# Kernel optimization log

Hardware: AMD Instinct MI355X
Metric: run time of the kernel (lower is better)

The kernel has to match this reference:

```python
import jax, jax.numpy as jnp
import numpy as np

NMS_PRE, NMS_POST, NMS_THRESH = 1024, 512, 0.7
B, A, FEAT = 4, 70400, 27648
BN_EPS = 1e-5


def _bev_iou(boxes):
    # boxes: [K, 7] (x, y, z, dx, dy, dz, ry); axis-aligned BEV IoU
    x, y, dx, dy = boxes[:, 0], boxes[:, 1], boxes[:, 3], boxes[:, 4]
    x1, x2 = x - 0.5 * dx, x + 0.5 * dx
    y1, y2 = y - 0.5 * dy, y + 0.5 * dy
    iw = jnp.clip(jnp.minimum(x2[:, None], x2[None, :]) - jnp.maximum(x1[:, None], x1[None, :]), 0.0)
    ih = jnp.clip(jnp.minimum(y2[:, None], y2[None, :]) - jnp.maximum(y1[:, None], y1[None, :]), 0.0)
    inter = iw * ih
    area = dx * dy
    return inter / jnp.clip(area[:, None] + area[None, :] - inter, 1e-6)


def _greedy_nms(boxes, thresh):
    # boxes sorted by score desc; returns keep mask [K]
    K = boxes.shape[0]
    iou = _bev_iou(boxes)
    idx = jnp.arange(K)

    def step(keep, i):
        sup = (iou[i] > thresh) & (idx > i) & keep[i]
        return keep & ~sup, None

    keep, _ = jax.lax.scan(step, jnp.ones(K, dtype=bool), jnp.arange(K))
    return keep


def _proposal_one(box, cls):
    # box: [A, 7], cls: [A, n_cls]  ->  padded rois [NPOST,7], scores [NPOST], labels [NPOST]
    score = jnp.max(cls, axis=-1)
    label = jnp.argmax(cls, axis=-1)
    top_score, top_idx = jax.lax.top_k(score, NMS_PRE)
    top_box = box[top_idx]
    keep = _greedy_nms(top_box, NMS_THRESH)
    # stable: kept entries first, preserving score order
    order = jnp.argsort(jnp.where(keep, jnp.arange(NMS_PRE), NMS_PRE + jnp.arange(NMS_PRE)))
    sel = order[:NMS_POST]
    valid = jnp.arange(NMS_POST) < jnp.minimum(jnp.sum(keep), NMS_POST)
    rois = jnp.where(valid[:, None], top_box[sel], 0.0)
    roi_score = jnp.where(valid, top_score[sel], 0.0)
    roi_label = jnp.where(valid, label[top_idx][sel], 0) + 1  # +1 as in module
    return rois, roi_score, roi_label


def _bn_relu(h, g, b):
    # eval-mode BN with running_mean=0, running_var=1
    return jax.nn.relu(h * (g / jnp.sqrt(1.0 + BN_EPS)) + b)


def _decode(reg, anchors):
    # ResidualCoder_v1.decode_torch
    xa, ya, za = anchors[..., 0], anchors[..., 1], anchors[..., 2]
    dxa, dya, dza, ra = anchors[..., 3], anchors[..., 4], anchors[..., 5], anchors[..., 6]
    xt, yt, zt = reg[..., 0], reg[..., 1], reg[..., 2]
    dxt, dyt, dzt, rt = reg[..., 3], reg[..., 4], reg[..., 5], reg[..., 6]
    diag = jnp.sqrt(dxa * dxa + dya * dya)
    return jnp.stack([
        xt * diag + xa, yt * diag + ya, zt * dza + za,
        jnp.exp(dxt) * dxa, jnp.exp(dyt) * dya, jnp.exp(dzt) * dza,
        rt + ra], axis=-1)


def _rotate_z(box, ang):
    # rotate x,y of box [..., 7] by ang [...]
    c, s = jnp.cos(ang), jnp.sin(ang)
    x = box[..., 0] * c - box[..., 1] * s
    y = box[..., 0] * s + box[..., 1] * c
    return jnp.concatenate([x[..., None], y[..., None], box[..., 2:]], axis=-1)


def reference(rpn_box_preds, rpn_cls_preds, pooled_features,
              Ws1, g1, b1, Ws2, g2, b2,
              Wc1, gc1, bc1, Wc2, gc2, bc2, Wc3, bc3,
              Wr1, gr1, br1, Wr2, gr2, br2, Wr3, br3):
    # proposal_layer: per-batch topk + NMS + padded scatter (vmapped)
    rois, roi_scores, roi_labels = jax.vmap(_proposal_one)(rpn_box_preds, rpn_cls_preds)

    # shared / cls / reg heads (1x1 Conv1d == per-roi MLP), dropout off (eval)
    x = _bn_relu(pooled_features @ Ws1.T, g1, b1)
    x = _bn_relu(x @ Ws2.T, g2, b2)
    c = _bn_relu(x @ Wc1.T, gc1, bc1)
    c = _bn_relu(c @ Wc2.T, gc2, bc2)
    cls_preds = c @ Wc3.T + bc3          # [B*NPOST, 1]
    r = _bn_relu(x @ Wr1.T, gr1, br1)
    r = _bn_relu(r @ Wr2.T, gr2, br2)
    reg_preds = r @ Wr3.T + br3          # [B*NPOST, 7]

    bsz = rois.shape[0]
    cls_preds = cls_preds.reshape(bsz, -1, cls_preds.shape[-1])
    reg_preds = reg_preds.reshape(bsz, -1, 7)

    # generate_predict_box: decode against detached rois with xyz zeroed
    anchors = jax.lax.stop_gradient(rois)
    anchors = anchors.at[..., 0:3].set(0.0)
    box_ct = _decode(reg_preds, anchors)
    box_preds = _rotate_z(box_ct, rois[..., 6])
    box_preds = jnp.concatenate([box_preds[..., 0:3] + rois[..., 0:3], box_preds[..., 3:]], axis=-1)

    return jnp.concatenate([cls_preds, box_preds, roi_scores[..., None]], axis=-1)  # [B, NPOST, 9]


def setup_inputs():
    key = jax.random.key(0)
    ks = jax.random.split(key, 32)
    u = jax.random.uniform(ks[0], (B, A, 7), dtype=jnp.float32)
    lo = jnp.array([0.0, -40.0, -2.0, 1.5, 1.4, 1.0, -3.14159], jnp.float32)
    hi = jnp.array([70.0, 40.0, 0.0, 4.5, 2.0, 2.0, 3.14159], jnp.float32)
    rpn_box_preds = lo + u * (hi - lo)
    rpn_cls_preds = jax.random.normal(ks[1], (B, A, 3), dtype=jnp.float32)
    pooled_features = jax.random.normal(ks[2], (B * NMS_POST, FEAT), dtype=jnp.float32) * 0.1

    def w(k, o, i, std=None):
        s = (1.0 / np.sqrt(i)) if std is None else std
        return jax.random.normal(k, (o, i), dtype=jnp.float32) * s

    d = dict(
        rpn_box_preds=rpn_box_preds, rpn_cls_preds=rpn_cls_preds, pooled_features=pooled_features,
        Ws1=w(ks[3], 256, FEAT), g1=jnp.ones(256), b1=jnp.zeros(256),
        Ws2=w(ks[4], 256, 256), g2=jnp.ones(256), b2=jnp.zeros(256),
        Wc1=w(ks[5], 256, 256), gc1=jnp.ones(256), bc1=jnp.zeros(256),
        Wc2=w(ks[6], 256, 256), gc2=jnp.ones(256), bc2=jnp.zeros(256),
        Wc3=w(ks[7], 1, 256), bc3=jnp.zeros(1),
        Wr1=w(ks[8], 256, 256), gr1=jnp.ones(256), br1=jnp.zeros(256),
        Wr2=w(ks[9], 256, 256), gr2=jnp.ones(256), br2=jnp.zeros(256),
        Wr3=w(ks[10], 7, 256, std=0.001), br3=jnp.zeros(7),
    )
    return d
```

## Files before the change

kernel.cpp:

```cpp
#include <hip/hip_runtime.h>
#include <cstdint>

typedef unsigned int u32;
typedef unsigned long long u64;
typedef unsigned short u16;

#define BATCH 4
#define A_CNT 70400
#define FEAT 27648
#define KSPLIT 16
#define KCHUNK 1728
#define NTILE_IT 27

typedef __attribute__((ext_vector_type(8))) short bf16x8;
typedef __attribute__((ext_vector_type(4))) float f32x4;
typedef __attribute__((ext_vector_type(2))) u32 u32x2;
typedef __attribute__((ext_vector_type(4))) u32 u32x4;

constexpr size_t OF_KEYS = 0;
constexpr size_t OF_TBOX = OF_KEYS + 1126400;
constexpr size_t OF_TSC  = OF_TBOX + 114688;
constexpr size_t OF_BX1  = OF_TSC + 16384;
constexpr size_t OF_BX2  = OF_BX1 + 16384;
constexpr size_t OF_BY1  = OF_BX2 + 16384;
constexpr size_t OF_BY2  = OF_BY1 + 16384;
constexpr size_t OF_BAR  = OF_BY2 + 16384;
constexpr size_t OF_MASK = OF_BAR + 16384;
constexpr size_t OF_ROIS = OF_MASK + 524288;
constexpr size_t OF_RSC  = OF_ROIS + 57344;
constexpr size_t OF_BSW  = OF_RSC + 8192;
constexpr size_t OF_PART = OF_BSW + 14155776;
constexpr size_t WS_NEED = OF_PART + 33554432;

__device__ __forceinline__ u32 keyOf(float f) {
  u32 u = __float_as_uint(f);
  return (u & 0x80000000u) ? ~u : (u | 0x80000000u);
}
__device__ __forceinline__ float keyToF(u32 k) {
  u32 u = (k & 0x80000000u) ? (k ^ 0x80000000u) : ~k;
  return __uint_as_float(u);
}
__device__ __forceinline__ u16 f2bf(float f) {
  u32 u = __float_as_uint(f);
  u32 r = 0x7FFFu + ((u >> 16) & 1u);
  return (u16)((u + r) >> 16);
}
__device__ __forceinline__ void gload_lds16(const void* g, void* l) {
  auto gp = reinterpret_cast<const __attribute__((address_space(1))) unsigned int*>(
      reinterpret_cast<uintptr_t>(g));
  auto lp = reinterpret_cast<__attribute__((address_space(3))) unsigned int*>(
      reinterpret_cast<uintptr_t>(l));
  __builtin_amdgcn_global_load_lds(gp, lp, 16, 0, 0);
}
__device__ __forceinline__ u64 shflx64(u64 v, int m) {
  u32 lo = (u32)v, hi = (u32)(v >> 32);
  lo = __shfl_xor(lo, m, 64);
  hi = __shfl_xor(hi, m, 64);
  return ((u64)hi << 32) | lo;
}
__device__ __forceinline__ u32x4 pack8(float4 a, float4 b) {
  u32x4 o;
  o.x = (u32)f2bf(a.x) | ((u32)f2bf(a.y) << 16);
  o.y = (u32)f2bf(a.z) | ((u32)f2bf(a.w) << 16);
  o.z = (u32)f2bf(b.x) | ((u32)f2bf(b.y) << 16);
  o.w = (u32)f2bf(b.z) | ((u32)f2bf(b.w) << 16);
  return o;
}

__global__ __launch_bounds__(1024) void k_fatA(const float* __restrict__ cls,
    const float* __restrict__ Ws1, u32* __restrict__ keys, u32* __restrict__ Bsw)
{
  int bid = blockIdx.x;
  int t = threadIdx.x;
  if (bid < 864) {
    u32 w = (u32)bid * 1024u + t;
    u32 tile = w >> 11;
    u32 rem = w & 2047u;
    u32 n = rem >> 3;
    u32 pq = (rem & 7u) << 4;
    u32 q0 = pq ^ ((n & 7u) << 4);
    u32 col0 = tile * 64u + (q0 >> 1);
    const float* src = Ws1 + (size_t)n * FEAT + col0;
    float4 f0 = *(const float4*)src;
    float4 f1 = *(const float4*)(src + 4);
    ((u32x4*)Bsw)[w] = pack8(f0, f1);
    return;
  }
  u32 g = (u32)(bid - 864) * 1024u + t;
  float s0 = cls[(size_t)g * 3 + 0];
  float s1 = cls[(size_t)g * 3 + 1];
  float s2 = cls[(size_t)g * 3 + 2];
  keys[g] = keyOf(fmaxf(s0, fmaxf(s1, s2)));
}

__global__ __launch_bounds__(1024) void k_big(const u32* __restrict__ keys,
    const float* __restrict__ boxes, const float* __restrict__ A,
    const u32* __restrict__ Bsw, float* __restrict__ part,
    float* __restrict__ tbox, float* __restrict__ tsc,
    float* __restrict__ bx1, float* __restrict__ bx2, float* __restrict__ by1,
    float* __restrict__ by2, float* __restrict__ bar)
{
  __shared__ __align__(16) char smem[98304];
  int bid = blockIdx.x;
  int t = threadIdx.x;
  if (bid < 4) {
    int b = bid;
    int lane = t & 63, wv = t >> 6;
    const u32* kb = keys + (size_t)b * A_CNT;
    u64* s = (u64*)smem;
    u32* partials = (u32*)(smem + 16384);
    u32* ccp = (u32*)(smem + 16448);
    u32 h[35];
#pragma unroll
    for (int j = 0; j < 35; ++j) {
      int g0 = t + ((2 * j) << 10);
      int g1 = t + ((2 * j + 1) << 10);
      u32 a = (g0 < A_CNT) ? (kb[g0] >> 16) : 0u;
      u32 c2 = (g1 < A_CNT) ? (kb[g1] >> 16) : 0u;
      h[j] = a | (c2 << 16);
    }
    if (t == 0) ccp[0] = 0u;
    u32 lo = 0, hi = 65536;
    while (hi - lo > 1) {
      u32 mid = (lo + hi) >> 1;
      u32 c = 0;
#pragma unroll
      for (int j = 0; j < 35; ++j) {
        c += ((h[j] & 0xFFFFu) >= mid) ? 1u : 0u;
        c += ((h[j] >> 16) >= mid) ? 1u : 0u;
      }
#pragma unroll
      for (int o = 32; o > 0; o >>= 1) c += __shfl_xor(c, o, 64);
      __syncthreads();
      if (lane == 0) partials[wv] = c;
      __syncthreads();
      u32 tot = 0;
#pragma unroll
      for (int w2 = 0; w2 < 16; ++w2) tot += partials[w2];
      if (tot >= 1024u) lo = mid; else hi = mid;
    }
    u32 kth = lo;
    __syncthreads();
    u32 kc = kb[t];
#pragma unroll 1
    for (int i = 0; i < 69; ++i) {
      int g = t + (i << 10);
      u32 k = kc;
      if (i < 68) {
        int gn = t + ((i + 1) << 10);
        kc = (gn < A_CNT) ? kb[gn] : 0u;
      }
      bool pass = (g < A_CNT) && ((k >> 16) >= kth);
      u64 mm = __ballot(pass);
      if (mm) {
        int leader = __ffsll((unsigned long long)mm) - 1;
        u32 base = 0;
        if (lane == leader) base = atomicAdd(ccp, (u32)__popcll(mm));
        base = __shfl(base, leader, 64);
        if (pass) {
          u32 pos = base + (u32)__popcll(mm & ((1ull << lane) - 1ull));
          if (pos < 2048u) s[pos] = ((u64)k << 32) | (u32)(~(u32)g);
        }
      }
    }
    __syncthreads();
    u32 m = ccp[0]; if (m > 2048u) m = 2048u;
    for (int e = t; e < 2048; e += 1024) if (e >= (int)m) s[e] = 0ull;
    __syncthreads();
    {
      u64 v0 = s[2 * t], v1 = s[2 * t + 1];
#pragma unroll
      for (u32 k = 2; k <= 128; k <<= 1) {
        bool desc = ((t & (k >> 1)) == 0);
#pragma unroll
        for (u32 j = (k >> 1); j >= 2; j >>= 1) {
          u32 mmk = j >> 1;
          u64 p0 = shflx64(v0, mmk);
          u64 p1 = shflx64(v1, mmk);
          bool up = ((t & mmk) == 0);
          bool mx = (desc == up);
          v0 = mx ? (v0 > p0 ? v0 : p0) : (v0 < p0 ? v0 : p0);
          v1 = mx ? (v1 > p1 ? v1 : p1) : (v1 < p1 ? v1 : p1);
        }
        if (desc ? (v0 < v1) : (v0 > v1)) { u64 tmp = v0; v0 = v1; v1 = tmp; }
      }
      s[2 * t] = v0; s[2 * t + 1] = v1;
      __syncthreads();
      for (u32 k = 256; k <= 2048; k <<= 1) {
        for (u32 j = k >> 1; j >= 128; j >>= 1) {
          for (int e = t; e < 2048; e += 1024) {
            u32 p = (u32)e ^ j;
            if (p > (u32)e) {
              bool d2 = ((e & k) == 0);
              u64 x = s[e], y = s[p];
              if (d2 ? (x < y) : (x > y)) { s[e] = y; s[p] = x; }
            }
          }
          __syncthreads();
        }
        u64 v0 = s[2 * t], v1 = s[2 * t + 1];
        bool desc = ((t & (k >> 1)) == 0);
#pragma unroll
        for (u32 j = 64; j >= 2; j >>= 1) {
          u32 mmk = j >> 1;
          u64 p0 = shflx64(v0, mmk);
          u64 p1 = shflx64(v1, mmk);
          bool up = ((t & mmk) == 0);
          bool mx = (desc == up);
          v0 = mx ? (v0 > p0 ? v0 : p0) : (v0 < p0 ? v0 : p0);
          v1 = mx ? (v1 > p1 ? v1 : p1) : (v1 < p1 ? v1 : p1);
        }
        if (desc ? (v0 < v1) : (v0 > v1)) { u64 tmp = v0; v0 = v1; v1 = tmp; }
        s[2 * t] = v0; s[2 * t + 1] = v1;
        __syncthreads();
      }
    }
    u64 comp = s[t];
    u32 kk = (u32)(comp >> 32);
    u32 a = ~(u32)(comp & 0xFFFFFFFFull);
    int o = b * 1024 + t;
    tsc[o] = keyToF(kk);
    const float* bp = boxes + ((size_t)b * A_CNT + a) * 7;
    float x = bp[0], y = bp[1], z = bp[2], dx = bp[3], dy = bp[4], dz = bp[5], rr = bp[6];
    float* tb = tbox + (size_t)o * 7;
    tb[0] = x; tb[1] = y; tb[2] = z; tb[3] = dx; tb[4] = dy; tb[5] = dz; tb[6] = rr;
    {
#pragma clang fp contract(off)
      bx1[o] = x - 0.5f * dx; bx2[o] = x + 0.5f * dx;
      by1[o] = y - 0.5f * dy; by2[o] = y + 0.5f * dy;
      bar[o] = dx * dy;
    }
    return;
  }
  int bid2 = bid - 4;
  int q = bid2 >> 3;
  int ks = (bid2 & 7) * 2 + (q >> 4);
  int mt = q & 15;
  int lane = t & 63, wvid = t >> 6;
  int row16 = lane & 15, kgrp = lane >> 4;
  int gm = wvid >> 2, gn = wvid & 3;

  f32x4 acc[2][4];
#pragma unroll
  for (int i = 0; i < 2; ++i)
#pragma unroll
    for (int j = 0; j < 4; ++j) acc[i][j] = (f32x4){0.f, 0.f, 0.f, 0.f};

  int arow = t >> 3;
  const float* ap_base = A + ((size_t)(mt * 128 + arow)) * FEAT + (size_t)ks * KCHUNK + (t & 7) * 8;
  int asw = (arow & 7) << 4;
  int awoff = arow * 128 + (((t & 7) * 16) ^ asw);
  const char* bsrc_base = (const char*)Bsw + ((size_t)(ks * NTILE_IT)) * 32768 + wvid * 2048 + lane * 16;
  int bdoff = wvid * 2048 + lane * 16;
  char* Abase = smem;
  char* Bbase = smem + 32768;

  int aoff[2][2], boff[4][2];
#pragma unroll
  for (int ksub = 0; ksub < 2; ++ksub) {
    int qq = ksub * 64 + kgrp * 16;
#pragma unroll
    for (int mf = 0; mf < 2; ++mf) {
      int row = gm * 32 + mf * 16 + row16;
      aoff[mf][ksub] = row * 128 + (qq ^ ((row & 7) << 4));
    }
#pragma unroll
    for (int nf = 0; nf < 4; ++nf) {
      int n = gn * 64 + nf * 16 + row16;
      boff[nf][ksub] = n * 128 + (qq ^ ((n & 7) << 4));
    }
  }

  {
    const float4* ap = (const float4*)ap_base;
    float4 ga0 = ap[0], ga1 = ap[1];
    *(u32x4*)(Abase + awoff) = pack8(ga0, ga1);
    gload_lds16(bsrc_base, Bbase + bdoff);
    gload_lds16(bsrc_base + 1024, Bbase + bdoff + 1024);
  }
  __syncthreads();

  for (int it = 0; it < NTILE_IT; ++it) {
    char* Acur = Abase + ((it & 1) ? 16384 : 0);
    char* Anxt = Abase + ((it & 1) ? 0 : 16384);
    char* Bcur = Bbase + ((it & 1) ? 32768 : 0);
    char* Bnxt = Bbase + ((it & 1) ? 0 : 32768);
    bool has = (it + 1 < NTILE_IT);
    float4 ga0, ga1;
    if (has) {
      const float4* ap = (const float4*)(ap_base + (it + 1) * 64);
      ga0 = ap[0]; ga1 = ap[1];
      const char* bs = bsrc_base + (size_t)(it + 1) * 32768;
      gload_lds16(bs, Bnxt + bdoff);
      gload_lds16(bs + 1024, Bnxt + bdoff + 1024);
    }
    bf16x8 af[2][2], bf[4][2];
#pragma unroll
    for (int ksub = 0; ksub < 2; ++ksub) {
#pragma unroll
      for (int mf = 0; mf < 2; ++mf) af[mf][ksub] = *(const bf16x8*)(Acur + aoff[mf][ksub]);
#pragma unroll
      for (int nf = 0; nf < 4; ++nf) bf[nf][ksub] = *(const bf16x8*)(Bcur + boff[nf][ksub]);
    }
#pragma unroll
    for (int ksub = 0; ksub < 2; ++ksub)
#pragma unroll
      for (int mf = 0; mf < 2; ++mf)
#pragma unroll
        for (int nf = 0; nf < 4; ++nf)
          acc[mf][nf] = __builtin_amdgcn_mfma_f32_16x16x32_bf16(af[mf][ksub], bf[nf][ksub], acc[mf][nf], 0, 0, 0);
    if (has)
      *(u32x4*)(Anxt + awoff) = pack8(ga0, ga1);
    __syncthreads();
  }
  float* pb = part + (size_t)ks * 524288;
#pragma unroll
  for (int mf = 0; mf < 2; ++mf) {
    int orow = mt * 128 + gm * 32 + mf * 16 + kgrp * 4;
#pragma unroll
    for (int nf = 0; nf < 4; ++nf) {
      int col = gn * 64 + nf * 16 + row16;
#pragma unroll
      for (int rr = 0; rr < 4; ++rr)
        pb[(size_t)(orow + rr) * 256 + col] = acc[mf][nf][rr];
    }
  }
}

__global__ __launch_bounds__(1024) void k_mask(const float* __restrict__ bx1,
    const float* __restrict__ bx2, const float* __restrict__ by1,
    const float* __restrict__ by2, const float* __restrict__ bar,
    u32* __restrict__ mask)
{
  __shared__ float csm[16][5][64];
  int tt = threadIdx.x;
  int ug = tt >> 6, ln = tt & 63;
  int unit = blockIdx.x * 16 + ug;
  int b = unit >> 8, cbk = (unit >> 4) & 15, rb = unit & 15;
  int o = b * 1024, jc0 = cbk * 64;
  int r = rb * 64 + ln;
  csm[ug][0][ln] = bx1[o + jc0 + ln];
  csm[ug][1][ln] = bx2[o + jc0 + ln];
  csm[ug][2][ln] = by1[o + jc0 + ln];
  csm[ug][3][ln] = by2[o + jc0 + ln];
  csm[ug][4][ln] = bar[o + jc0 + ln];
  __syncthreads();
  float rx1 = bx1[o + r], rx2 = bx2[o + r], ry1 = by1[o + r], ry2 = by2[o + r], rar = bar[o + r];
  u32 w0 = 0, w1 = 0;
  {
#pragma clang fp contract(off)
    for (int c = 0; c < 64; ++c) {
      int jc = jc0 + c;
      float iw = fminf(rx2, csm[ug][1][c]) - fmaxf(rx1, csm[ug][0][c]); iw = fmaxf(iw, 0.0f);
      float ih = fminf(ry2, csm[ug][3][c]) - fmaxf(ry1, csm[ug][2][c]); ih = fmaxf(ih, 0.0f);
      float inter = iw * ih;
      float den = fmaxf(rar + csm[ug][4][c] - inter, 1e-6f);
      float iou = inter / den;
      if ((iou > 0.7f) && (jc > r)) {
        if (c < 32) w0 |= 1u << c; else w1 |= 1u << (c - 32);
      }
    }
  }
  mask[((size_t)(o + r)) * 32 + cbk * 2 + 0] = w0;
  mask[((size_t)(o + r)) * 32 + cbk * 2 + 1] = w1;
}

__global__ __launch_bounds__(64) void k_nms(const u32* __restrict__ mask,
    const float* __restrict__ tbox, const float* __restrict__ tsc,
    float* __restrict__ rois, float* __restrict__ rsc)
{
  int b = blockIdx.x;
  int lane = threadIdx.x;
  int el = lane & 31;
  const u32* M = mask + (size_t)b * 1024 * 32;
  u32 R = 0;
  u32 cur[32], nxt[32];
#pragma unroll
  for (int i = 0; i < 32; ++i) cur[i] = M[(size_t)(i * 32 + el)];
#pragma unroll 1
  for (int c = 0; c < 32; ++c) {
    if (c < 31) {
      int nb = (c + 1) * 1024 + el;
#pragma unroll
      for (int i = 0; i < 32; ++i) nxt[i] = M[(size_t)(nb + i * 32)];
    }
    u32 w = R;
#pragma unroll
    for (int i = 0; i < 32; ++i) w |= ((w >> i) & 1u) ? 0u : cur[i];
    u32 wfin = __shfl(w, c, 64);
#pragma unroll
    for (int i = 0; i < 32; ++i) R |= ((wfin >> i) & 1u) ? 0u : cur[i];
#pragma unroll
    for (int i = 0; i < 32; ++i) cur[i] = nxt[i];
  }
  u32 keepw = (lane < 32) ? ~R : 0u;
  int c = __popc(keepw);
  int pre = c;
  for (int d = 1; d < 64; d <<= 1) {
    int v = __shfl_up(pre, d, 64);
    if (lane >= d) pre += v;
  }
  int total = __shfl(pre, 31, 64);
  int base = pre - c;
  if (lane < 32) {
    u32 w = keepw;
    int rank = base;
    while (w) {
      int bit = __ffs(w) - 1;
      w &= w - 1;
      if (rank < 512) {
        int r = lane * 32 + bit;
        const float* tb = tbox + ((size_t)b * 1024 + r) * 7;
        float* rp = rois + ((size_t)b * 512 + rank) * 7;
        rp[0] = tb[0]; rp[1] = tb[1]; rp[2] = tb[2]; rp[3] = tb[3];
        rp[4] = tb[4]; rp[5] = tb[5]; rp[6] = tb[6];
        rsc[b * 512 + rank] = tsc[b * 1024 + r];
      }
      rank++;
    }
  }
  for (int z = total + lane; z < 512; z += 64) {
    float* rp = rois + ((size_t)b * 512 + z) * 7;
    rp[0] = rp[1] = rp[2] = rp[3] = rp[4] = rp[5] = rp[6] = 0.0f;
    rsc[b * 512 + z] = 0.0f;
  }
}

__device__ __forceinline__ void layer4(const float (*IN)[256], const float* __restrict__ W,
    const float* __restrict__ g, const float* __restrict__ bb, float (*OUT)[256], int t, int h)
{
  float acc[4] = {0, 0, 0, 0};
  const float* Wrow = W + (size_t)t * 256;
  for (int k = 0; k < 256; k += 4) {
    float4 w4 = *(const float4*)&Wrow[k];
#pragma unroll
    for (int r = 0; r < 4; ++r) {
      float4 xv = *(const float4*)&IN[h * 4 + r][k];
      acc[r] = fmaf(xv.x, w4.x, acc[r]);
      acc[r] = fmaf(xv.y, w4.y, acc[r]);
      acc[r] = fmaf(xv.z, w4.z, acc[r]);
      acc[r] = fmaf(xv.w, w4.w, acc[r]);
    }
  }
  float sc = g[t] / sqrtf(1.0f + 1e-5f);
  float bv = bb[t];
#pragma unroll
  for (int r = 0; r < 4; ++r)
    OUT[h * 4 + r][t] = fmaxf(fmaf(acc[r], sc, bv), 0.0f);
}

__global__ __launch_bounds__(512) void k_chain(const float* __restrict__ part,
    const float* __restrict__ Ws2, const float* __restrict__ Wc1, const float* __restrict__ Wc2,
    const float* __restrict__ Wr1, const float* __restrict__ Wr2,
    const float* __restrict__ g1, const float* __restrict__ b1,
    const float* __restrict__ g2, const float* __restrict__ b2,
    const float* __restrict__ gc1, const float* __restrict__ bc1,
    const float* __restrict__ gc2, const float* __restrict__ bc2,
    const float* __restrict__ gr1, const float* __restrict__ br1,
    const float* __restrict__ gr2, const float* __restrict__ br2,
    const float* __restrict__ Wc3, const float* __restrict__ bc3,
    const float* __restrict__ Wr3, const float* __restrict__ br3,
    const float* __restrict__ rois, const float* __restrict__ rsc,
    float* __restrict__ out)
{
  int bid = blockIdx.x, tid = threadIdx.x;
  int t = tid & 255, h = tid >> 8;
  __shared__ __align__(16) float bufX[8][256];
  __shared__ __align__(16) float bufY[8][256];
  __shared__ __align__(16) float bufC[8][256];
  __shared__ __align__(16) float bufR[8][256];
  __shared__ float hd[64];
  {
    float sc = g1[t] / sqrtf(1.0f + 1e-5f);
    float bv = b1[t];
#pragma unroll
    for (int r = 0; r < 4; ++r) {
      int row = h * 4 + r;
      float s = 0.f;
#pragma unroll
      for (int ks = 0; ks < KSPLIT; ++ks)
        s += part[(size_t)ks * 524288 + (size_t)(bid * 8 + row) * 256 + t];
      bufX[row][t] = fmaxf(fmaf(s, sc, bv), 0.0f);
    }
  }
  __syncthreads();
  layer4(bufX, Ws2, g2, b2, bufY, t, h);
  __syncthreads();
  layer4(bufY, Wc1, gc1, bc1, bufC, t, h);
  layer4(bufY, Wr1, gr1, br1, bufR, t, h);
  __syncthreads();
  layer4(bufC, Wc2, gc2, bc2, bufX, t, h);
  layer4(bufR, Wr2, gr2, br2, bufY, t, h);
  __syncthreads();
  int wv = tid >> 6, ln = tid & 63;
  for (int task = wv; task < 64; task += 8) {
    float p;
    if (task < 8) {
      float4 yv = *(const float4*)&bufX[task][ln * 4];
      float4 w4 = ((const float4*)Wc3)[ln];
      p = yv.x * w4.x + yv.y * w4.y + yv.z * w4.z + yv.w * w4.w;
    } else {
      int i = task - 8, row = i / 7, j = i % 7;
      float4 yv = *(const float4*)&bufY[row][ln * 4];
      float4 w4 = ((const float4*)(Wr3 + j * 256))[ln];
      p = yv.x * w4.x + yv.y * w4.y + yv.z * w4.z + yv.w * w4.w;
    }
#pragma unroll
    for (int off = 32; off > 0; off >>= 1) p += __shfl_xor(p, off, 64);
    if (ln == 0) hd[task] = p;
  }
  __syncthreads();
  if (tid < 8) {
    int m = bid * 8 + tid;
    float clsv = hd[tid] + bc3[0];
    float rg[7];
#pragma unroll
    for (int j = 0; j < 7; ++j) rg[j] = hd[8 + tid * 7 + j] + br3[j];
    const float* R = rois + (size_t)m * 7;
    float rx = R[0], ry = R[1], rz = R[2], dxa = R[3], dya = R[4], dza = R[5], ra = R[6];
    float diag = sqrtf(dxa * dxa + dya * dya);
    float x = rg[0] * diag, y = rg[1] * diag, z = rg[2] * dza;
    float ex = expf(rg[3]) * dxa, ey = expf(rg[4]) * dya, ez = expf(rg[5]) * dza;
    float hr = rg[6] + ra;
    float cc = cosf(ra), sn = sinf(ra);
    float xr = x * cc - y * sn, yr = x * sn + y * cc;
    float* O = out + (size_t)m * 9;
    O[0] = clsv; O[1] = xr + rx; O[2] = yr + ry; O[3] = z + rz;
    O[4] = ex; O[5] = ey; O[6] = ez; O[7] = hr; O[8] = rsc[m];
  }
}

extern "C" void kernel_launch(void* const* d_in, const int* in_sizes, int n_in,
                              void* d_out, int out_size, void* d_ws, size_t ws_size,
                              hipStream_t stream)
{
  const float* rpn_box = (const float*)d_in[0];
  const float* rpn_cls = (const float*)d_in[1];
  const float* pooled  = (const float*)d_in[2];
  const float* Ws1 = (const float*)d_in[3];
  const float* g1  = (const float*)d_in[4];
  const float* b1  = (const float*)d_in[5];
  const float* Ws2 = (const float*)d_in[6];
  const float* g2  = (const float*)d_in[7];
  const float* b2  = (const float*)d_in[8];
  const float* Wc1 = (const float*)d_in[9];
  const float* gc1 = (const float*)d_in[10];
  const float* bc1 = (const float*)d_in[11];
  const float* Wc2 = (const float*)d_in[12];
  const float* gc2 = (const float*)d_in[13];
  const float* bc2 = (const float*)d_in[14];
  const float* Wc3 = (const float*)d_in[15];
  const float* bc3 = (const float*)d_in[16];
  const float* Wr1 = (const float*)d_in[17];
  const float* gr1 = (const float*)d_in[18];
  const float* br1 = (const float*)d_in[19];
  const float* Wr2 = (const float*)d_in[20];
  const float* gr2 = (const float*)d_in[21];
  const float* br2 = (const float*)d_in[22];
  const float* Wr3 = (const float*)d_in[23];
  const float* br3 = (const float*)d_in[24];

  if (ws_size < WS_NEED) return;

  char* ws = (char*)d_ws;
  u32* keys = (u32*)(ws + OF_KEYS);
  float* tbox = (float*)(ws + OF_TBOX);
  float* tsc  = (float*)(ws + OF_TSC);
  float* bx1 = (float*)(ws + OF_BX1);
  float* bx2 = (float*)(ws + OF_BX2);
  float* by1 = (float*)(ws + OF_BY1);
  float* by2 = (float*)(ws + OF_BY2);
  float* bar = (float*)(ws + OF_BAR);
  u32* mask = (u32*)(ws + OF_MASK);
  float* roisb = (float*)(ws + OF_ROIS);
  float* rscb  = (float*)(ws + OF_RSC);
  u32* Bsw = (u32*)(ws + OF_BSW);
  float* part = (float*)(ws + OF_PART);

  k_fatA<<<1139, 1024, 0, stream>>>(rpn_cls, Ws1, keys, Bsw);
  k_big<<<260, 1024, 0, stream>>>(keys, rpn_box, pooled, Bsw, part,
                                  tbox, tsc, bx1, bx2, by1, by2, bar);
  k_mask<<<64, 1024, 0, stream>>>(bx1, bx2, by1, by2, bar, mask);
  k_nms<<<4, 64, 0, stream>>>(mask, tbox, tsc, roisb, rscb);
  k_chain<<<256, 512, 0, stream>>>(part, Ws2, Wc1, Wc2, Wr1, Wr2,
                                   g1, b1, g2, b2, gc1, bc1, gc2, bc2,
                                   gr1, br1, gr2, br2, Wc3, bc3, Wr3, br3,
                                   roisb, rscb, (float*)d_out);
}
```

Measured before the change: 247.2 us.

## Triple-buffer B tiles with prefetch distance two and ping-pong NMS mask buffers

The split-K GEMM loop now prefetches the B tile two iterations ahead into a triple-buffered LDS region (shared memory grown to 128 KB). It replaces __syncthreads with explicit waitcnt on vmcnt and lgkmcnt plus s_barrier, so later loads stay in flight across the barrier. The NMS chunk loop is unrolled by two with ping-pong register buffers, removing the 32-element copy, and splits the OR reduction into four independent chains. The larger LDS footprint may reduce occupancy, and the hand-written waitcnt counts must match the real number of outstanding loads or the results will be wrong.

After: 242.7 us (median of 2 runs). No clear change (-1.8%).

```diff
diff --git a/kernel.cpp b/kernel.cpp
--- a/kernel.cpp
+++ b/kernel.cpp
@@ -100,7 +100,7 @@
     float* __restrict__ bx1, float* __restrict__ bx2, float* __restrict__ by1,
     float* __restrict__ by2, float* __restrict__ bar)
 {
-  __shared__ __align__(16) char smem[98304];
+  __shared__ __align__(16) char smem[131072];
   int bid = blockIdx.x;
   int t = threadIdx.x;
   if (bid < 4) {
@@ -271,28 +271,37 @@
     }
   }
 
+  float4 gaold0, gaold1;
   {
-    const float4* ap = (const float4*)ap_base;
-    float4 ga0 = ap[0], ga1 = ap[1];
-    *(u32x4*)(Abase + awoff) = pack8(ga0, ga1);
+    const float4* ap0 = (const float4*)ap_base;
+    float4 a00 = ap0[0], a01 = ap0[1];
     gload_lds16(bsrc_base, Bbase + bdoff);
     gload_lds16(bsrc_base + 1024, Bbase + bdoff + 1024);
-  }
-  __syncthreads();
-
+    const float4* ap1 = (const float4*)(ap_base + 64);
+    gaold0 = ap1[0]; gaold1 = ap1[1];
+    const char* bs1 = bsrc_base + 32768;
+    gload_lds16(bs1, Bbase + 32768 + bdoff);
+    gload_lds16(bs1 + 1024, Bbase + 32768 + bdoff + 1024);
+    *(u32x4*)(Abase + awoff) = pack8(a00, a01);
+    asm volatile("s_waitcnt lgkmcnt(0)" ::: "memory");
+    asm volatile("s_waitcnt vmcnt(4)" ::: "memory");
+    __builtin_amdgcn_sched_barrier(0);
+    __builtin_amdgcn_s_barrier();
+  }
+
+#pragma unroll 1
   for (int it = 0; it < NTILE_IT; ++it) {
-    char* Acur = Abase + ((it & 1) ? 16384 : 0);
-    char* Anxt = Abase + ((it & 1) ? 0 : 16384);
-    char* Bcur = Bbase + ((it & 1) ? 32768 : 0);
-    char* Bnxt = Bbase + ((it & 1) ? 0 : 32768);
-    bool has = (it + 1 < NTILE_IT);
-    float4 ga0, ga1;
-    if (has) {
-      const float4* ap = (const float4*)(ap_base + (it + 1) * 64);
-      ga0 = ap[0]; ga1 = ap[1];
-      const char* bs = bsrc_base + (size_t)(it + 1) * 32768;
-      gload_lds16(bs, Bnxt + bdoff);
-      gload_lds16(bs + 1024, Bnxt + bdoff + 1024);
+    char* Acur = Abase + ((it & 1) << 14);
+    char* Bcur = Bbase + (it % 3) * 32768;
+    bool pf = (it + 2 < NTILE_IT);
+    float4 gn0, gn1;
+    if (pf) {
+      const float4* ap = (const float4*)(ap_base + (it + 2) * 64);
+      gn0 = ap[0]; gn1 = ap[1];
+      const char* bs = bsrc_base + (size_t)(it + 2) * 32768;
+      char* Bn = Bbase + ((it + 2) % 3) * 32768;
+      gload_lds16(bs, Bn + bdoff);
+      gload_lds16(bs + 1024, Bn + bdoff + 1024);
     }
     bf16x8 af[2][2], bf[4][2];
 #pragma unroll
@@ -309,9 +318,16 @@
 #pragma unroll
         for (int nf = 0; nf < 4; ++nf)
           acc[mf][nf] = __builtin_amdgcn_mfma_f32_16x16x32_bf16(af[mf][ksub], bf[nf][ksub], acc[mf][nf], 0, 0, 0);
-    if (has)
-      *(u32x4*)(Anxt + awoff) = pack8(ga0, ga1);
-    __syncthreads();
+    if (it + 1 < NTILE_IT) {
+      char* An = Abase + (((it + 1) & 1) << 14);
+      *(u32x4*)(An + awoff) = pack8(gaold0, gaold1);
+      gaold0 = gn0; gaold1 = gn1;
+      asm volatile("s_waitcnt lgkmcnt(0)" ::: "memory");
+      if (pf) asm volatile("s_waitcnt vmcnt(4)" ::: "memory");
+      else    asm volatile("s_waitcnt vmcnt(0)" ::: "memory");
+      __builtin_amdgcn_sched_barrier(0);
+      __builtin_amdgcn_s_barrier();
+    }
   }
   float* pb = part + (size_t)ks * 524288;
 #pragma unroll
@@ -365,6 +381,27 @@
   mask[((size_t)(o + r)) * 32 + cbk * 2 + 1] = w1;
 }
 
+#define CHUNK_STEP(CUR, NXT, C) do {                                            \
+    if ((C) + 1 < 32) {                                                         \
+      int nb = ((C) + 1) * 1024 + el;                                           \
+      _Pragma("unroll")                                                         \
+      for (int i = 0; i < 32; ++i) NXT[i] = M[(size_t)(nb + i * 32)];           \
+    }                                                                           \
+    u32 w = R;                                                                  \
+    _Pragma("unroll")                                                           \
+    for (int i = 0; i < 32; ++i) w |= ((w >> i) & 1u) ? 0u : CUR[i];            \
+    u32 wfin = __shfl(w, (C), 64);                                              \
+    u32 m0 = 0, m1 = 0, m2 = 0, m3 = 0;                                         \
+    _Pragma("unroll")                                                           \
+    for (int i = 0; i < 32; i += 4) {                                           \
+      m0 |= ((wfin >> (i + 0)) & 1u) ? 0u : CUR[i + 0];                         \
+      m1 |= ((wfin >> (i + 1)) & 1u) ? 0u : CUR[i + 1];                         \
+      m2 |= ((wfin >> (i + 2)) & 1u) ? 0u : CUR[i + 2];                         \
+      m3 |= ((wfin >> (i + 3)) & 1u) ? 0u : CUR[i + 3];                         \
+    }                                                                           \
+    R |= (m0 | m1) | (m2 | m3);                                                 \
+  } while (0)
+
 __global__ __launch_bounds__(64) void k_nms(const u32* __restrict__ mask,
     const float* __restrict__ tbox, const float* __restrict__ tsc,
     float* __restrict__ rois, float* __restrict__ rsc)
@@ -374,24 +411,13 @@
   int el = lane & 31;
   const u32* M = mask + (size_t)b * 1024 * 32;
   u32 R = 0;
-  u32 cur[32], nxt[32];
-#pragma unroll
-  for (int i = 0; i < 32; ++i) cur[i] = M[(size_t)(i * 32 + el)];
+  u32 bufA[32], bufB[32];
+#pragma unroll
+  for (int i = 0; i < 32; ++i) bufA[i] = M[(size_t)(i * 32 + el)];
 #pragma unroll 1
-  for (int c = 0; c < 32; ++c) {
-    if (c < 31) {
-      int nb = (c + 1) * 1024 + el;
-#pragma unroll
-      for (int i = 0; i < 32; ++i) nxt[i] = M[(size_t)(nb + i * 32)];
-    }
-    u32 w = R;
-#pragma unroll
-    for (int i = 0; i < 32; ++i) w |= ((w >> i) & 1u) ? 0u : cur[i];
-    u32 wfin = __shfl(w, c, 64);
-#pragma unroll
-    for (int i = 0; i < 32; ++i) R |= ((wfin >> i) & 1u) ? 0u : cur[i];
-#pragma unroll
-    for (int i = 0; i < 32; ++i) cur[i] = nxt[i];
+  for (int c = 0; c < 32; c += 2) {
+    CHUNK_STEP(bufA, bufB, c);
+    CHUNK_STEP(bufB, bufA, c + 1);
   }
   u32 keepw = (lane < 32) ? ~R : 0u;
   int c = __popc(keepw);
```
